# Performance work log

Hardware: AMD Instinct MI355X
Metric: run time of the kernel (lower is better)

Reference implementation:

```python
import jax, jax.numpy as jnp
import numpy as np

B, A, NBH, F, G, H = 8, 512, 64, 128, 50, 8
DH = F // H
CUTOFF = 5.0


def setup_inputs() -> dict:
    key = jax.random.key(0)
    ks = jax.random.split(key, 13)
    x = jax.random.normal(ks[0], (B, A, F), jnp.float32)
    e = jax.random.normal(ks[1], (B, A, F), jnp.float32)
    t = jax.random.normal(ks[2], (B, F), jnp.float32)
    # distances in [0, 1.2*cutoff] so some pairs fall outside the cutoff
    r_ij = jax.random.uniform(ks[3], (B, A, NBH), jnp.float32) * (1.2 * CUTOFF)
    f_ij = jax.random.normal(ks[4], (B, A, NBH, G), jnp.float32)
    neighbors = jax.random.randint(ks[5], (B, A, NBH), 0, A, jnp.int32)
    neighbor_mask = jax.random.randint(ks[6], (B, A, NBH), 0, 2, jnp.int32).astype(bool)
    sF = 1.0 / np.sqrt(F).astype(np.float32)
    W_filt = jax.random.normal(ks[7], (G, F), jnp.float32) * (1.0 / np.sqrt(G).astype(np.float32))
    b_filt = jnp.zeros((F,), jnp.float32)
    Wq = jax.random.normal(ks[8], (F, F), jnp.float32) * sF
    Wk = jax.random.normal(ks[9], (F, F), jnp.float32) * sF
    Wv = jax.random.normal(ks[10], (F, F), jnp.float32) * sF
    Wo = jax.random.normal(ks[11], (F, F), jnp.float32) * sF
    bo = jnp.zeros((F,), jnp.float32)
    return dict(e=e, x=x, t=t, r_ij=r_ij, f_ij=f_ij,
                W_filt=W_filt, b_filt=b_filt, Wq=Wq, Wk=Wk, Wv=Wv, Wo=Wo, bo=bo,
                neighbors=neighbors, neighbor_mask=neighbor_mask)


def reference(e, x, t, r_ij, f_ij, W_filt, b_filt, Wq, Wk, Wv, Wo, bo,
              neighbors, neighbor_mask):
    # ---- filter network + cosine cutoff: W (B, A, NBH, F) ----
    W = f_ij @ W_filt + b_filt
    C = 0.5 * (jnp.cos(jnp.pi * r_ij / CUTOFF) + 1.0)
    C = C * (r_ij < CUTOFF).astype(x.dtype)           # (B, A, NBH)
    W = W * C[..., None]

    # ---- neighbor gather: nbh (B, A, NBH, F) ----
    bidx = jnp.arange(B)[:, None, None]
    nbh = x[bidx, neighbors]                           # irregular gather
    nbh = nbh * W                                      # filter-modulated messages

    # ---- EgoAttention: central atom queries its neighbors ----
    q = (x @ Wq).reshape(B, A, H, DH)                  # bahd
    k = (nbh @ Wk).reshape(B, A, NBH, H, DH)           # banhd
    v = (nbh @ Wv).reshape(B, A, NBH, H, DH)
    scale = np.float32(1.0 / np.sqrt(DH))
    scores = jnp.einsum('bahd,banhd->bahn', q, k) * scale
    scores = jnp.where(neighbor_mask[:, :, None, :], scores, jnp.float32(-1e9))
    attn = jax.nn.softmax(scores, axis=-1)             # over neighbors
    msg = jnp.einsum('bahn,banhd->bahd', attn, v).reshape(B, A, F)
    v_out = msg @ Wo + bo

    # ---- residual (apply_transition_function=False branch) ----
    return x + v_out
```

## Files before the change

kernel.cpp:

```cpp
#include <hip/hip_runtime.h>
#include <math.h>

#define BB 8
#define AA 512
#define NBH 64
#define FF 128
#define GG 50
#define CUTOFF 5.0f

typedef __attribute__((ext_vector_type(8)))  short bf16x8;
typedef __attribute__((ext_vector_type(4)))  float f32x4;
typedef __attribute__((ext_vector_type(16))) float f32x16;

#define MST 136

#define WKV_ELEMS (4*8*64*8)
#define WQO_ELEMS (8*4*64*8)
#define WF_ELEMS  (4*4*64*8)
#define XB_ELEMS  (BB*AA*FF)

__device__ __forceinline__ short f2bf(float f) {
    union { float f; unsigned u; } v; v.f = f;
    unsigned r = v.u + 0x7fffu + ((v.u >> 16) & 1u);
    return (short)(r >> 16);
}
__device__ __forceinline__ short f2bf_fast(float f) {
    return (short)((__float_as_uint(f) + 0x8000u) >> 16);
}
__device__ __forceinline__ unsigned int pk2bf(float a, float b) {
    unsigned int ua = __float_as_uint(a) + 0x8000u;
    unsigned int ub = __float_as_uint(b) + 0x8000u;
    return __builtin_amdgcn_perm(ub, ua, 0x07060302u);
}
__device__ __forceinline__ bf16x8 ld_f8_bfpk(const float* p) {
    const float2* p2 = (const float2*)p;
    float2 a = p2[0], b = p2[1], c = p2[2], d = p2[3];
    union { unsigned int u[4]; bf16x8 v; } r;
    r.u[0] = pk2bf(a.x, a.y);
    r.u[1] = pk2bf(b.x, b.y);
    r.u[2] = pk2bf(c.x, c.y);
    r.u[3] = pk2bf(d.x, d.y);
    return r.v;
}
__device__ __forceinline__ int swz(int n) { return ((n >> 3) & 3) << 3; }

__device__ __forceinline__ float row16_sum(float x) {
    int t;
    t = __builtin_amdgcn_update_dpp(0, __float_as_int(x), 0x128, 0xf, 0xf, true); x += __int_as_float(t);
    t = __builtin_amdgcn_update_dpp(0, __float_as_int(x), 0x124, 0xf, 0xf, true); x += __int_as_float(t);
    t = __builtin_amdgcn_update_dpp(0, __float_as_int(x), 0x122, 0xf, 0xf, true); x += __int_as_float(t);
    t = __builtin_amdgcn_update_dpp(0, __float_as_int(x), 0x121, 0xf, 0xf, true); x += __int_as_float(t);
    return x;
}

__global__ void prep_kernel(const float* __restrict__ Wk,
                            const float* __restrict__ Wv,
                            const float* __restrict__ Wq,
                            const float* __restrict__ Wo,
                            const float* __restrict__ Wf,
                            const float* __restrict__ b_filt,
                            const float* __restrict__ x,
                            short* __restrict__ ws)
{
    int gid = blockIdx.x * blockDim.x + threadIdx.x;
    if (gid < 2 * WKV_ELEMS) {
        const float* src = (gid < WKV_ELEMS) ? Wk : Wv;
        int idx = gid & (WKV_ELEMS - 1);
        int j = idx & 7, l = (idx >> 3) & 63, rest = idx >> 9;
        int s = rest & 7, w = rest >> 3;
        int k = 16 * s + ((l >> 5) << 3) + j;
        int n = 32 * w + (l & 31);
        ws[gid] = f2bf(src[k * FF + n]);
    } else if (gid < 2 * WKV_ELEMS + 2 * WQO_ELEMS) {
        int idx2 = gid - 2 * WKV_ELEMS;
        const float* src = (idx2 < WQO_ELEMS) ? Wq : Wo;
        int idx = idx2 & (WQO_ELEMS - 1);
        int j = idx & 7, l = (idx >> 3) & 63, rest = idx >> 9;
        int s = rest & 3, c = rest >> 2;
        int k = 32 * s + (l >> 4) * 8 + j;
        int n = 16 * c + (l & 15);
        ws[gid] = f2bf(src[k * FF + n]);
    } else if (gid < 2 * WKV_ELEMS + 2 * WQO_ELEMS + WF_ELEMS) {
        int idx = gid - 2 * WKV_ELEMS - 2 * WQO_ELEMS;
        int j = idx & 7, l = (idx >> 3) & 63, rest = idx >> 9;
        int s = rest & 3, w = rest >> 2;
        int k = 16 * s + ((l >> 5) << 3) + j;
        int n = 32 * w + (l & 31);
        float v = (k < GG) ? Wf[k * FF + n] : (k == GG ? b_filt[n] : 0.0f);
        ws[gid] = f2bf(v);
    } else {
        int idx = gid - 2 * WKV_ELEMS - 2 * WQO_ELEMS - WF_ELEMS;
        ws[gid] = f2bf(x[idx]);
    }
}

__global__ __launch_bounds__(256, 4)
void tdt_main(const float* __restrict__ x,
              const float* __restrict__ r_ij,
              const float* __restrict__ f_ij,
              const float* __restrict__ bo,
              const int*   __restrict__ neighbors,
              const int*   __restrict__ nmask,
              const short* __restrict__ WkB,
              const short* __restrict__ WvB,
              const short* __restrict__ WqB,
              const short* __restrict__ WoB,
              const short* __restrict__ WfB,
              const short* __restrict__ xB,
              float* __restrict__ out)
{
    const int ba   = blockIdx.x;
    const int b    = ba >> 9;
    const int tid  = threadIdx.x;
    const int lane = tid & 63;
    const int w    = tid >> 6;
    const int l15  = lane & 15;
    const int quad = lane >> 4;
    const int l31  = lane & 31;
    const int khalf = (lane >> 5) << 3;
    const int w5_4  = (lane >> 5) * 4;

    __shared__ short M_s[NBH * MST];
    __shared__ short msg_bf[FF];

    const float* xrow = x + (size_t)ba * FF;
    const unsigned short* xbu = (const unsigned short*)xB + (size_t)b * AA * FF;
    const size_t bao = (size_t)ba;

    int   nbr_reg = neighbors[bao * NBH + lane];
    float C_reg;
    {
        float r = r_ij[bao * NBH + lane];
        float c = 0.5f * (__cosf((float)M_PI * r * (1.0f / CUTOFF)) + 1.0f);
        C_reg = (r < CUTOFF) ? c : 0.0f;
    }
    unsigned long long mask64 = __ballot(nmask[bao * NBH + lane] != 0);

    float qvm;
    {
        const short* xbrow = &xB[(size_t)ba * FF];
        bf16x8 xa[4];
#pragma unroll
        for (int s = 0; s < 4; ++s)
            xa[s] = *(const bf16x8*)&xbrow[32 * s + quad * 8];
        float qv0, qv1;
#pragma unroll
        for (int ct = 0; ct < 2; ++ct) {
            int cg = 2 * w + ct;
            f32x4 z = {0.f, 0.f, 0.f, 0.f};
#pragma unroll
            for (int s = 0; s < 4; ++s) {
                bf16x8 bq = *(const bf16x8*)&WqB[((cg * 4 + s) * 64 + lane) * 8];
                z = __builtin_amdgcn_mfma_f32_16x16x32_bf16(xa[s], bq, z, 0, 0, 0);
            }
            if (ct == 0) qv0 = z[0]; else qv1 = z[0];
        }
        qvm = (((lane >> 4) & 1) ? qv1 : qv0) * 0.25f;
    }

    {
        const float* fm0 = f_ij + bao * (size_t)(NBH * GG) + (size_t)l31 * GG;
        int c = 32 * w + l31;
#pragma unroll
        for (int mt = 0; mt < 2; ++mt) {
            f32x16 wacc;
#pragma unroll
            for (int r = 0; r < 16; ++r) wacc[r] = 0.0f;
            const float* fm = fm0 + mt * 32 * GG;
#pragma unroll
            for (int s = 0; s < 4; ++s) {
                bf16x8 bfw = *(const bf16x8*)&WfB[((w * 4 + s) * 64 + lane) * 8];
                bf16x8 fa;
                if (s < 3) {
                    fa = ld_f8_bfpk(fm + 16 * s + khalf);
                } else {
#pragma unroll
                    for (int jj = 0; jj < 8; ++jj) fa[jj] = 0;
                    if (lane < 32) {
                        fa[0] = f2bf_fast(fm[48]);
                        fa[1] = f2bf_fast(fm[49]);
                        fa[2] = (short)0x3F80;
                    }
                }
                wacc = __builtin_amdgcn_mfma_f32_32x32x16_bf16(fa, bfw, wacc, 0, 0, 0);
            }
#pragma unroll
            for (int r = 0; r < 16; ++r) {
                int   n   = 32 * mt + (r & 3) + 8 * (r >> 2) + w5_4;
                int   nbn = __shfl(nbr_reg, n, 64);
                float cn  = __shfl(C_reg, n, 64);
                float xv  = __uint_as_float((unsigned)xbu[(size_t)nbn * FF + c] << 16);
                M_s[n * MST + (c ^ swz(n))] = f2bf_fast(wacc[r] * cn * xv);
            }
        }
    }
    __syncthreads();

    float sum = 0.0f, acc = 0.0f;
#pragma unroll
    for (int mt = 0; mt < 2; ++mt) {
        int m = 32 * mt + l31;
        f32x16 kacc, vacc;
#pragma unroll
        for (int r = 0; r < 16; ++r) { kacc[r] = 0.0f; vacc[r] = 0.0f; }
#pragma unroll
        for (int s = 0; s < 8; ++s) {
            bf16x8 ma = *(const bf16x8*)&M_s[m * MST + ((16 * s + khalf) ^ swz(m))];
            bf16x8 bk = *(const bf16x8*)&WkB[((w * 8 + s) * 64 + lane) * 8];
            bf16x8 bv = *(const bf16x8*)&WvB[((w * 8 + s) * 64 + lane) * 8];
            kacc = __builtin_amdgcn_mfma_f32_32x32x16_bf16(ma, bk, kacc, 0, 0, 0);
            vacc = __builtin_amdgcn_mfma_f32_32x32x16_bf16(ma, bv, vacc, 0, 0, 0);
        }
#pragma unroll
        for (int r = 0; r < 16; ++r) {
            float sr = row16_sum(kacc[r] * qvm);
            int   n  = 32 * mt + (r & 3) + 8 * (r >> 2) + w5_4;
            float e  = ((mask64 >> n) & 1ull) ? __expf(sr) : 0.0f;
            sum += e;
            acc  = fmaf(e, vacc[r], acc);
        }
    }
    sum += __shfl_xor(sum, 32, 64);
    acc += __shfl_xor(acc, 32, 64);
    if (lane < 32) msg_bf[32 * w + l31] = f2bf_fast(acc / sum);
    __syncthreads();

    {
        bf16x8 mga[4];
#pragma unroll
        for (int s = 0; s < 4; ++s)
            mga[s] = *(const bf16x8*)&msg_bf[s * 32 + quad * 8];
#pragma unroll
        for (int ct = 0; ct < 2; ++ct) {
            int cg = 2 * w + ct;
            f32x4 z = {0.f, 0.f, 0.f, 0.f};
#pragma unroll
            for (int s = 0; s < 4; ++s) {
                bf16x8 bw = *(const bf16x8*)&WoB[((cg * 4 + s) * 64 + lane) * 8];
                z = __builtin_amdgcn_mfma_f32_16x16x32_bf16(mga[s], bw, z, 0, 0, 0);
            }
            if (quad == 0) {
                int col = cg * 16 + l15;
                out[bao * FF + col] = z[0] + xrow[col] + bo[col];
            }
        }
    }
}

extern "C" void kernel_launch(void* const* d_in, const int* in_sizes, int n_in,
                              void* d_out, int out_size, void* d_ws, size_t ws_size,
                              hipStream_t stream) {
    const float* x      = (const float*)d_in[1];
    const float* r_ij   = (const float*)d_in[3];
    const float* f_ij   = (const float*)d_in[4];
    const float* W_filt = (const float*)d_in[5];
    const float* b_filt = (const float*)d_in[6];
    const float* Wq     = (const float*)d_in[7];
    const float* Wk     = (const float*)d_in[8];
    const float* Wv     = (const float*)d_in[9];
    const float* Wo     = (const float*)d_in[10];
    const float* bo     = (const float*)d_in[11];
    const int*   nbr    = (const int*)d_in[12];
    const int*   msk    = (const int*)d_in[13];
    float* out = (float*)d_out;

    short* ws  = (short*)d_ws;
    short* WkB = ws;
    short* WvB = ws + WKV_ELEMS;
    short* WqB = ws + 2 * WKV_ELEMS;
    short* WoB = ws + 2 * WKV_ELEMS + WQO_ELEMS;
    short* WfB = ws + 2 * WKV_ELEMS + 2 * WQO_ELEMS;
    short* xB  = ws + 2 * WKV_ELEMS + 2 * WQO_ELEMS + WF_ELEMS;

    int prep_total = 2 * WKV_ELEMS + 2 * WQO_ELEMS + WF_ELEMS + XB_ELEMS;
    hipLaunchKernelGGL(prep_kernel, dim3(prep_total / 256), dim3(256), 0, stream,
                       Wk, Wv, Wq, Wo, W_filt, b_filt, x, ws);
    hipLaunchKernelGGL(tdt_main, dim3(BB * AA), dim3(256), 0, stream,
                       x, r_ij, f_ij, bo, nbr, msk,
                       WkB, WvB, WqB, WoB, WfB, xB, out);
}
```

Baseline: 162.6 us.

## Fold query into key projection to compute scores directly from messages

Precomputes, for each atom and head, the vector Wk·q_h (scaled) in the prep kernel, giving a per-atom 128x8 bf16 matrix. The main kernel then gets attention scores with one MFMA over the message tile against this vector instead of computing full K, multiplying by q and doing DPP row reductions. This also removes the Wq MFMA stage from the main kernel. In exchange the prep kernel does an FP32 scalar Wq and Wk matvec per atom and writes an extra 8 MB-scale bf16 buffer that the main kernel reads per block.

```diff
diff --git a/kernel.cpp b/kernel.cpp
--- a/kernel.cpp
+++ b/kernel.cpp
@@ -14,10 +14,14 @@
 
 #define MST 136
 
-#define WKV_ELEMS (4*8*64*8)
-#define WQO_ELEMS (8*4*64*8)
-#define WF_ELEMS  (4*4*64*8)
-#define XB_ELEMS  (BB*AA*FF)
+#define WV_OFF   0
+#define WO_OFF   16384
+#define WF_OFF   32768
+#define XB_OFF   40960
+#define KQ_OFF   565248
+#define PACK_ELEMS 565248
+#define PACK_BLOCKS (PACK_ELEMS / 256)
+#define QK_BLOCKS  1024
 
 __device__ __forceinline__ short f2bf(float f) {
     union { float f; unsigned u; } v; v.f = f;
@@ -44,53 +48,93 @@
 }
 __device__ __forceinline__ int swz(int n) { return ((n >> 3) & 3) << 3; }
 
-__device__ __forceinline__ float row16_sum(float x) {
-    int t;
-    t = __builtin_amdgcn_update_dpp(0, __float_as_int(x), 0x128, 0xf, 0xf, true); x += __int_as_float(t);
-    t = __builtin_amdgcn_update_dpp(0, __float_as_int(x), 0x124, 0xf, 0xf, true); x += __int_as_float(t);
-    t = __builtin_amdgcn_update_dpp(0, __float_as_int(x), 0x122, 0xf, 0xf, true); x += __int_as_float(t);
-    t = __builtin_amdgcn_update_dpp(0, __float_as_int(x), 0x121, 0xf, 0xf, true); x += __int_as_float(t);
-    return x;
-}
-
-__global__ void prep_kernel(const float* __restrict__ Wk,
+__global__ void prep_kernel(const float* __restrict__ Wq,
+                            const float* __restrict__ Wk,
                             const float* __restrict__ Wv,
-                            const float* __restrict__ Wq,
                             const float* __restrict__ Wo,
                             const float* __restrict__ Wf,
                             const float* __restrict__ b_filt,
                             const float* __restrict__ x,
                             short* __restrict__ ws)
 {
-    int gid = blockIdx.x * blockDim.x + threadIdx.x;
-    if (gid < 2 * WKV_ELEMS) {
-        const float* src = (gid < WKV_ELEMS) ? Wk : Wv;
-        int idx = gid & (WKV_ELEMS - 1);
-        int j = idx & 7, l = (idx >> 3) & 63, rest = idx >> 9;
-        int s = rest & 7, w = rest >> 3;
-        int k = 16 * s + ((l >> 5) << 3) + j;
-        int n = 32 * w + (l & 31);
-        ws[gid] = f2bf(src[k * FF + n]);
-    } else if (gid < 2 * WKV_ELEMS + 2 * WQO_ELEMS) {
-        int idx2 = gid - 2 * WKV_ELEMS;
-        const float* src = (idx2 < WQO_ELEMS) ? Wq : Wo;
-        int idx = idx2 & (WQO_ELEMS - 1);
-        int j = idx & 7, l = (idx >> 3) & 63, rest = idx >> 9;
-        int s = rest & 3, c = rest >> 2;
-        int k = 32 * s + (l >> 4) * 8 + j;
-        int n = 16 * c + (l & 15);
-        ws[gid] = f2bf(src[k * FF + n]);
-    } else if (gid < 2 * WKV_ELEMS + 2 * WQO_ELEMS + WF_ELEMS) {
-        int idx = gid - 2 * WKV_ELEMS - 2 * WQO_ELEMS;
-        int j = idx & 7, l = (idx >> 3) & 63, rest = idx >> 9;
-        int s = rest & 3, w = rest >> 2;
-        int k = 16 * s + ((l >> 5) << 3) + j;
-        int n = 32 * w + (l & 31);
-        float v = (k < GG) ? Wf[k * FF + n] : (k == GG ? b_filt[n] : 0.0f);
-        ws[gid] = f2bf(v);
-    } else {
-        int idx = gid - 2 * WKV_ELEMS - 2 * WQO_ELEMS - WF_ELEMS;
-        ws[gid] = f2bf(x[idx]);
+    const int bid = blockIdx.x;
+    const int tid = threadIdx.x;
+
+    if (bid < PACK_BLOCKS) {
+        int gid = bid * 256 + tid;
+        if (gid < 16384) {
+            int idx = gid;
+            int j = idx & 7, l = (idx >> 3) & 63, rest = idx >> 9;
+            int s = rest & 7, w = rest >> 3;
+            int k = 16 * s + ((l >> 5) << 3) + j;
+            int n = 32 * w + (l & 31);
+            ws[WV_OFF + gid] = f2bf(Wv[k * FF + n]);
+        } else if (gid < 32768) {
+            int idx = gid - 16384;
+            int j = idx & 7, l = (idx >> 3) & 63, rest = idx >> 9;
+            int s = rest & 3, c = rest >> 2;
+            int k = 32 * s + (l >> 4) * 8 + j;
+            int n = 16 * c + (l & 15);
+            ws[WO_OFF + idx] = f2bf(Wo[k * FF + n]);
+        } else if (gid < 40960) {
+            int idx = gid - 32768;
+            int j = idx & 7, l = (idx >> 3) & 63, rest = idx >> 9;
+            int s = rest & 3, w = rest >> 2;
+            int k = 16 * s + ((l >> 5) << 3) + j;
+            int n = 32 * w + (l & 31);
+            float v = (k < GG) ? Wf[k * FF + n] : (k == GG ? b_filt[n] : 0.0f);
+            ws[WF_OFF + idx] = f2bf(v);
+        } else {
+            int idx = gid - XB_OFF;
+            ws[XB_OFF + idx] = f2bf(x[idx]);
+        }
+        return;
+    }
+
+    __shared__ float xq[4][256];
+    const int w    = tid >> 6;
+    const int lane = tid & 63;
+    const int a    = (bid - PACK_BLOCKS) * 4 + w;
+    float* xl = &xq[w][0];
+    float* ql = &xq[w][128];
+
+    const float* xa = x + (size_t)a * FF;
+    xl[lane]      = xa[lane];
+    xl[lane + 64] = xa[lane + 64];
+    __syncthreads();
+
+    {
+        float a0 = 0.0f, a1 = 0.0f;
+#pragma unroll 8
+        for (int i = 0; i < FF; ++i) {
+            float xv = xl[i];
+            a0 = fmaf(xv, Wq[i * FF + lane], a0);
+            a1 = fmaf(xv, Wq[i * FF + lane + 64], a1);
+        }
+        ql[lane]      = a0 * 0.25f;
+        ql[lane + 64] = a1 * 0.25f;
+    }
+    __syncthreads();
+
+    short* kqa = ws + KQ_OFF + (size_t)a * 1024;
+#pragma unroll
+    for (int h = 0; h < 8; ++h) {
+        const float4* qh = (const float4*)&ql[16 * h];
+        float4 q0 = qh[0], q1 = qh[1], q2 = qh[2], q3 = qh[3];
+        const float4* wr0 = (const float4*)&Wk[(size_t)lane * FF + 16 * h];
+        const float4* wr1 = (const float4*)&Wk[(size_t)(lane + 64) * FF + 16 * h];
+        float s0 = 0.0f, s1 = 0.0f;
+        float4 t;
+        t = wr0[0]; s0 = fmaf(t.x,q0.x,fmaf(t.y,q0.y,fmaf(t.z,q0.z,fmaf(t.w,q0.w,s0))));
+        t = wr0[1]; s0 = fmaf(t.x,q1.x,fmaf(t.y,q1.y,fmaf(t.z,q1.z,fmaf(t.w,q1.w,s0))));
+        t = wr0[2]; s0 = fmaf(t.x,q2.x,fmaf(t.y,q2.y,fmaf(t.z,q2.z,fmaf(t.w,q2.w,s0))));
+        t = wr0[3]; s0 = fmaf(t.x,q3.x,fmaf(t.y,q3.y,fmaf(t.z,q3.z,fmaf(t.w,q3.w,s0))));
+        t = wr1[0]; s1 = fmaf(t.x,q0.x,fmaf(t.y,q0.y,fmaf(t.z,q0.z,fmaf(t.w,q0.w,s1))));
+        t = wr1[1]; s1 = fmaf(t.x,q1.x,fmaf(t.y,q1.y,fmaf(t.z,q1.z,fmaf(t.w,q1.w,s1))));
+        t = wr1[2]; s1 = fmaf(t.x,q2.x,fmaf(t.y,q2.y,fmaf(t.z,q2.z,fmaf(t.w,q2.w,s1))));
+        t = wr1[3]; s1 = fmaf(t.x,q3.x,fmaf(t.y,q3.y,fmaf(t.z,q3.z,fmaf(t.w,q3.w,s1))));
+        kqa[h * 128 + lane]      = f2bf(s0);
+        kqa[h * 128 + lane + 64] = f2bf(s1);
     }
 }
 
@@ -101,12 +145,11 @@
               const float* __restrict__ bo,
               const int*   __restrict__ neighbors,
               const int*   __restrict__ nmask,
-              const short* __restrict__ WkB,
               const short* __restrict__ WvB,
-              const short* __restrict__ WqB,
               const short* __restrict__ WoB,
               const short* __restrict__ WfB,
               const short* __restrict__ xB,
+              const short* __restrict__ kqc,
               float* __restrict__ out)
 {
     const int ba   = blockIdx.x;
@@ -136,28 +179,6 @@
     }
     unsigned long long mask64 = __ballot(nmask[bao * NBH + lane] != 0);
 
-    float qvm;
-    {
-        const short* xbrow = &xB[(size_t)ba * FF];
-        bf16x8 xa[4];
-#pragma unroll
-        for (int s = 0; s < 4; ++s)
-            xa[s] = *(const bf16x8*)&xbrow[32 * s + quad * 8];
-        float qv0, qv1;
-#pragma unroll
-        for (int ct = 0; ct < 2; ++ct) {
-            int cg = 2 * w + ct;
-            f32x4 z = {0.f, 0.f, 0.f, 0.f};
-#pragma unroll
-            for (int s = 0; s < 4; ++s) {
-                bf16x8 bq = *(const bf16x8*)&WqB[((cg * 4 + s) * 64 + lane) * 8];
-                z = __builtin_amdgcn_mfma_f32_16x16x32_bf16(xa[s], bq, z, 0, 0, 0);
-            }
-            if (ct == 0) qv0 = z[0]; else qv1 = z[0];
-        }
-        qvm = (((lane >> 4) & 1) ? qv1 : qv0) * 0.25f;
-    }
-
     {
         const float* fm0 = f_ij + bao * (size_t)(NBH * GG) + (size_t)l31 * GG;
         int c = 32 * w + l31;
@@ -197,25 +218,25 @@
     __syncthreads();
 
     float sum = 0.0f, acc = 0.0f;
+    const short* kqa = kqc + (size_t)ba * 1024 + (size_t)(2 * w + ((lane >> 4) & 1)) * 128;
 #pragma unroll
     for (int mt = 0; mt < 2; ++mt) {
         int m = 32 * mt + l31;
-        f32x16 kacc, vacc;
-#pragma unroll
-        for (int r = 0; r < 16; ++r) { kacc[r] = 0.0f; vacc[r] = 0.0f; }
+        f32x16 sacc, vacc;
+#pragma unroll
+        for (int r = 0; r < 16; ++r) { sacc[r] = 0.0f; vacc[r] = 0.0f; }
 #pragma unroll
         for (int s = 0; s < 8; ++s) {
             bf16x8 ma = *(const bf16x8*)&M_s[m * MST + ((16 * s + khalf) ^ swz(m))];
-            bf16x8 bk = *(const bf16x8*)&WkB[((w * 8 + s) * 64 + lane) * 8];
+            bf16x8 bq = *(const bf16x8*)&kqa[16 * s + khalf];
             bf16x8 bv = *(const bf16x8*)&WvB[((w * 8 + s) * 64 + lane) * 8];
-            kacc = __builtin_amdgcn_mfma_f32_32x32x16_bf16(ma, bk, kacc, 0, 0, 0);
+            sacc = __builtin_amdgcn_mfma_f32_32x32x16_bf16(ma, bq, sacc, 0, 0, 0);
             vacc = __builtin_amdgcn_mfma_f32_32x32x16_bf16(ma, bv, vacc, 0, 0, 0);
         }
 #pragma unroll
         for (int r = 0; r < 16; ++r) {
-            float sr = row16_sum(kacc[r] * qvm);
-            int   n  = 32 * mt + (r & 3) + 8 * (r >> 2) + w5_4;
-            float e  = ((mask64 >> n) & 1ull) ? __expf(sr) : 0.0f;
+            int   n = 32 * mt + (r & 3) + 8 * (r >> 2) + w5_4;
+            float e = ((mask64 >> n) & 1ull) ? __expf(sacc[r]) : 0.0f;
             sum += e;
             acc  = fmaf(e, vacc[r], acc);
         }
@@ -265,17 +286,15 @@
     float* out = (float*)d_out;
 
     short* ws  = (short*)d_ws;
-    short* WkB = ws;
-    short* WvB = ws + WKV_ELEMS;
-    short* WqB = ws + 2 * WKV_ELEMS;
-    short* WoB = ws + 2 * WKV_ELEMS + WQO_ELEMS;
-    short* WfB = ws + 2 * WKV_ELEMS + 2 * WQO_ELEMS;
-    short* xB  = ws + 2 * WKV_ELEMS + 2 * WQO_ELEMS + WF_ELEMS;
-
-    int prep_total = 2 * WKV_ELEMS + 2 * WQO_ELEMS + WF_ELEMS + XB_ELEMS;
-    hipLaunchKernelGGL(prep_kernel, dim3(prep_total / 256), dim3(256), 0, stream,
-                       Wk, Wv, Wq, Wo, W_filt, b_filt, x, ws);
+    short* WvB = ws + WV_OFF;
+    short* WoB = ws + WO_OFF;
+    short* WfB = ws + WF_OFF;
+    short* xB  = ws + XB_OFF;
+    short* kqc = ws + KQ_OFF;
+
+    hipLaunchKernelGGL(prep_kernel, dim3(PACK_BLOCKS + QK_BLOCKS), dim3(256), 0, stream,
+                       Wq, Wk, Wv, Wo, W_filt, b_filt, x, ws);
     hipLaunchKernelGGL(tdt_main, dim3(BB * AA), dim3(256), 0, stream,
                        x, r_ij, f_ij, bo, nbr, msk,
-                       WkB, WvB, WqB, WoB, WfB, xB, out);
-}
+                       WvB, WoB, WfB, xB, kqc, out);
+}
```

Result: slower. 211.2 us (+29.9%).
